# Kernel optimization log

Hardware: AMD Instinct MI355X
Metric: run time of the kernel (lower is better)

The kernel has to match this reference:

```python
import jax, jax.numpy as jnp
import numpy as np

N = 50000      # num_nodes
R = 12         # num_relations
RL = 2 * R + 1 # relation slots in each RGCN layer
D = 128        # embedding_dim
H = 128        # hidden_layer_size
B = 4          # num_bases
E = 320000     # num_edges


def _xavier(key, shape):
    fan_in, fan_out = shape[-2], shape[-1]
    lim = np.sqrt(6.0 / (fan_in + fan_out)).astype(np.float32)
    return jax.random.uniform(key, shape, jnp.float32, -lim, lim)


def setup_inputs() -> dict:
    key = jax.random.key(0)
    ks = jax.random.split(key, 12)
    edge_index = jax.random.randint(ks[0], (2, E), 0, N)
    edge_type = jax.random.randint(ks[1], (E,), 0, R)
    neg_tail = jax.random.randint(ks[2], (E,), 0, N)  # corrupted tails for BCE loss
    entity_embedding = _xavier(ks[3], (N, D))
    entity_bias = jnp.zeros((1, D), jnp.float32)
    bases1 = _xavier(ks[4], (B, D, H))
    comp1 = _xavier(ks[5], (RL, B))
    bias1 = jnp.zeros((H,), jnp.float32)
    bases2 = _xavier(ks[6], (B, H, D))
    comp2 = _xavier(ks[7], (RL, B))
    bias2 = jnp.zeros((D,), jnp.float32)
    rel_emb = _xavier(ks[8], (R, D))
    return {
        "entity_embedding": entity_embedding, "entity_bias": entity_bias,
        "bases1": bases1, "comp1": comp1, "bias1": bias1,
        "bases2": bases2, "comp2": comp2, "bias2": bias2,
        "rel_emb": rel_emb,
        "edge_index": edge_index, "edge_type": edge_type, "neg_tail": neg_tail,
    }


def rgcn_layer(x, edge_index, edge_type, bases, comp, bias):
    # Basis-decomposed relational conv: W_r = sum_b comp[r,b] * bases[b]
    # Project once through bases, then combine per-edge with comp[edge_type].
    src, dst = edge_index[0], edge_index[1]
    hb = jnp.einsum('ni,bio->nbo', x, bases)            # [N, B, out]
    c = comp[edge_type]                                  # [E, B]
    msg = jnp.einsum('eb,ebo->eo', c, hb[src])           # [E, out]
    n_edges = edge_type.shape[0]
    deg = jax.ops.segment_sum(jnp.ones((n_edges,), x.dtype), dst, num_segments=N)
    agg = jax.ops.segment_sum(msg, dst, num_segments=N)  # scatter-add aggregation
    return agg / jnp.maximum(deg, 1.0)[:, None] + bias


def reference(entity_embedding, entity_bias, bases1, comp1, bias1,
              bases2, comp2, bias2, rel_emb, edge_index, edge_type, neg_tail):
    x = jax.nn.relu(entity_embedding + entity_bias)
    x = jax.nn.relu(rgcn_layer(x, edge_index, edge_type, bases1, comp1, bias1))
    x = rgcn_layer(x, edge_index, edge_type, bases2, comp2, bias2)
    # DistMult decoding over the graph triples (h, r, t)
    h, t = edge_index[0], edge_index[1]
    re = rel_emb[edge_type]                              # [E, D]
    pred_logits = jnp.sum(x[h] * re * x[t], axis=-1)     # [E]
    neg_logits = jnp.sum(x[h] * re * x[neg_tail], axis=-1)
    loss = 0.5 * (jnp.mean(-jax.nn.log_sigmoid(pred_logits))
                  + jnp.mean(-jax.nn.log_sigmoid(-neg_logits)))
    roc_auc = jnp.mean((pred_logits > neg_logits).astype(jnp.float32))
    return pred_logits, loss, roc_auc
```

## Files before the change

kernel.cpp:

```cpp
#include <hip/hip_runtime.h>

typedef unsigned short ushort_t;
typedef __attribute__((ext_vector_type(8))) short short8;
typedef __attribute__((ext_vector_type(4))) float f32x4;

#define N_NODES 50000
#define NBASE   4
#define N_EDGE  320000
#define DM_BLOCKS 2048
#define N_GROUPS (N_EDGE / 8)
#define SCAN_BLOCKS 49
#define LDSB_STRIDE 136
#define FILL_B (N_EDGE / 256)
#define X0_B   (N_NODES * 128 / 256)

#define C_COMP1 0
#define C_COMP2 100
#define C_BIAS1 200
#define C_BIAS2 328
#define C_REL   456
#define C_EBIAS 1992
#define C_TOTAL 2120

__device__ __forceinline__ float bf2f(ushort_t u) {
    union { unsigned int i; float f; } v; v.i = ((unsigned int)u) << 16; return v.f;
}
__device__ __forceinline__ ushort_t f2bf(float f) {
    union { float f; unsigned int i; } v; v.f = f;
    unsigned int u = v.i;
    u = (u + 0x7FFFu + ((u >> 16) & 1u)) >> 16;
    return (ushort_t)u;
}
__device__ __forceinline__ float readf(const void* p, int i, int isbf) {
    return isbf ? bf2f(((const ushort_t*)p)[i]) : ((const float*)p)[i];
}
__device__ __forceinline__ float softplus(float x) {
    if (x > 20.f) return x;
    if (x < -20.f) return expf(x);
    return log1pf(expf(x));
}

__global__ void k_prepcnt(const ushort_t* __restrict__ emb, int* __restrict__ flag,
                          const void* comp1, const void* comp2, const void* b1, const void* b2,
                          const void* rel, const void* eb, float* __restrict__ canon,
                          const int* __restrict__ ei, int* __restrict__ cnt) {
    if (blockIdx.x == 0) {
        __shared__ int c;
        if (threadIdx.x == 0) c = 0;
        __syncthreads();
        int e = (emb[threadIdx.x] >> 7) & 0xFF;
        if (e >= 100 && e <= 126) atomicAdd(&c, 1);
        __syncthreads();
        if (threadIdx.x == 0) *flag = (c >= 200) ? 1 : 0;
        int isbf = (c >= 200) ? 1 : 0;
        for (int i = threadIdx.x; i < C_TOTAL; i += blockDim.x) {
            float v;
            if      (i < C_COMP2) v = readf(comp1, i - C_COMP1, isbf);
            else if (i < C_BIAS1) v = readf(comp2, i - C_COMP2, isbf);
            else if (i < C_BIAS2) v = readf(b1,    i - C_BIAS1, isbf);
            else if (i < C_REL)   v = readf(b2,    i - C_BIAS2, isbf);
            else if (i < C_EBIAS) v = readf(rel,   i - C_REL,   isbf);
            else                  v = readf(eb,    i - C_EBIAS, isbf);
            canon[i] = v;
        }
    } else {
        int e = (blockIdx.x - 1) * 256 + threadIdx.x;
        if (e < N_EDGE) atomicAdd(&cnt[ei[N_EDGE + e]], 1);
    }
}

__global__ void k_scan1(const int* __restrict__ cnt, int* __restrict__ ptr,
                        int* __restrict__ bsum) {
    __shared__ int s[1024];
    int t = threadIdx.x;
    int i = blockIdx.x * 1024 + t;
    int v = (i < N_NODES) ? cnt[i] : 0;
    s[t] = v;
    __syncthreads();
    for (int off = 1; off < 1024; off <<= 1) {
        int u = (t >= off) ? s[t - off] : 0;
        __syncthreads();
        s[t] += u;
        __syncthreads();
    }
    if (i < N_NODES) ptr[i] = s[t] - v;
    if (t == 1023) bsum[blockIdx.x] = s[1023];
}

__global__ void k_scan2(const int* __restrict__ bsum, int* __restrict__ boff) {
    int t = threadIdx.x;
    int v = (t < SCAN_BLOCKS) ? bsum[t] : 0;
    int orig = v;
    #pragma unroll
    for (int off = 1; off < 64; off <<= 1) {
        int u = __shfl_up(v, off);
        if (t >= off) v += u;
    }
    boff[t] = v - orig;
}

__global__ void k_scan3(int* __restrict__ ptr, int* __restrict__ cursor,
                        const int* __restrict__ boff) {
    int t = threadIdx.x;
    int i = blockIdx.x * 1024 + t;
    if (i < N_NODES) {
        int p = ptr[i] + boff[blockIdx.x];
        ptr[i] = p;
        cursor[i] = p;
    }
    if (blockIdx.x == 0 && t == 0) ptr[N_NODES] = N_EDGE;
}

__global__ void k_fillinit(const int* __restrict__ ei, const int* __restrict__ et,
                           int* __restrict__ cursor, unsigned int* __restrict__ packed,
                           const void* __restrict__ bases1, ushort_t* __restrict__ btK1,
                           const void* __restrict__ bases2, ushort_t* __restrict__ btK2,
                           const void* __restrict__ emb, const float* __restrict__ canon,
                           ushort_t* __restrict__ x, const int* __restrict__ flag) {
    int bid = blockIdx.x;
    if (bid < FILL_B) {
        int e = bid * 256 + threadIdx.x;
        int dst = ei[N_EDGE + e];
        int pos = atomicAdd(&cursor[dst], 1);
        packed[pos] = (unsigned int)(ei[e] & 0xFFFF) | ((unsigned int)et[e] << 16);
    } else if (bid < FILL_B + 512) {
        int isbf = *flag;
        int rb = bid - FILL_B;
        const void* bases = (rb < 256) ? bases1 : bases2;
        ushort_t* btK = (rb < 256) ? btK1 : btK2;
        int idx = (rb & 255) * 256 + threadIdx.x;
        int b = idx >> 14, i = (idx >> 7) & 127, o = idx & 127;
        btK[(size_t)o * 512 + (b << 7) + i] = f2bf(readf(bases, idx, isbf));
    } else {
        int isbf = *flag;
        int i = (bid - FILL_B - 512) * 256 + threadIdx.x;
        if (i < N_NODES * 128) {
            float v = readf(emb, i, isbf) + canon[C_EBIAS + (i & 127)];
            x[i] = f2bf(fmaxf(v, 0.f));
        }
    }
}

__global__ void k_agg2(const ushort_t* __restrict__ x, const int* __restrict__ ptr,
                       const unsigned int* __restrict__ packed, const float* __restrict__ compf,
                       ushort_t* __restrict__ y) {
    __shared__ float sc[100];
    int tid = threadIdx.x;
    for (int i = tid; i < 100; i += 256) sc[i] = compf[i];
    __syncthreads();
    int m = blockIdx.x * 4 + (tid >> 6);
    int lane = tid & 63;
    int o2 = lane << 1;
    int beg = ptr[m], end = ptr[m + 1];
    float l0 = 0.f, l1 = 0.f, l2 = 0.f, l3 = 0.f;
    float h0 = 0.f, h1 = 0.f, h2 = 0.f, h3 = 0.f;
    int i = beg;
    for (; i + 8 <= end; i += 8) {
        unsigned int p[8], wv[8];
        #pragma unroll
        for (int j = 0; j < 8; ++j) p[j] = packed[i + j];
        #pragma unroll
        for (int j = 0; j < 8; ++j)
            wv[j] = *(const unsigned int*)(x + (size_t)(p[j] & 0xFFFFu) * 128 + o2);
        #pragma unroll
        for (int j = 0; j < 8; ++j) {
            const float* c = sc + (p[j] >> 16) * 4;
            float vl = bf2f((ushort_t)wv[j]), vh = bf2f((ushort_t)(wv[j] >> 16));
            l0 += c[0] * vl; l1 += c[1] * vl; l2 += c[2] * vl; l3 += c[3] * vl;
            h0 += c[0] * vh; h1 += c[1] * vh; h2 += c[2] * vh; h3 += c[3] * vh;
        }
    }
    for (; i < end; ++i) {
        unsigned int p0 = packed[i];
        unsigned int w0 = *(const unsigned int*)(x + (size_t)(p0 & 0xFFFFu) * 128 + o2);
        const float* c0 = sc + (p0 >> 16) * 4;
        float vl = bf2f((ushort_t)w0), vh = bf2f((ushort_t)(w0 >> 16));
        l0 += c0[0] * vl; l1 += c0[1] * vl; l2 += c0[2] * vl; l3 += c0[3] * vl;
        h0 += c0[0] * vh; h1 += c0[1] * vh; h2 += c0[2] * vh; h3 += c0[3] * vh;
    }
    unsigned int* yp = (unsigned int*)(y + (size_t)m * 512 + o2);
    yp[0]   = (unsigned int)f2bf(l0) | ((unsigned int)f2bf(h0) << 16);
    yp[64]  = (unsigned int)f2bf(l1) | ((unsigned int)f2bf(h1) << 16);
    yp[128] = (unsigned int)f2bf(l2) | ((unsigned int)f2bf(h2) << 16);
    yp[192] = (unsigned int)f2bf(l3) | ((unsigned int)f2bf(h3) << 16);
}

__global__ __launch_bounds__(256) void
k_gemm512(const ushort_t* __restrict__ y, const ushort_t* __restrict__ btK,
          const int* __restrict__ cnt, const float* __restrict__ canon,
          ushort_t* __restrict__ xout, int cbias, int dorelu) {
    __shared__ ushort_t bs[128 * LDSB_STRIDE];
    int tid = threadIdx.x;
    int lane = tid & 63, w = tid >> 6;
    int r = lane & 15, q = lane >> 4;
    int m0 = blockIdx.x * 128;
    f32x4 acc[2][8] = {};
    int row0 = m0 + w * 32 + r;
    int row1 = row0 + 16;
    int cr0 = (row0 < N_NODES) ? row0 : (N_NODES - 1);
    int cr1 = (row1 < N_NODES) ? row1 : (N_NODES - 1);
    const ushort_t* ar0 = y + (size_t)cr0 * 512;
    const ushort_t* ar1 = y + (size_t)cr1 * 512;

    for (int c = 0; c < 4; ++c) {
        __syncthreads();
        {
            int o = tid >> 4;
            int j = (tid & 15) << 3;
            #pragma unroll
            for (int s = 0; s < 8; ++s, o += 16) {
                short8 v = *(const short8*)(btK + (size_t)o * 512 + c * 128 + j);
                *(short8*)(bs + o * LDSB_STRIDE + j) = v;
            }
        }
        __syncthreads();
        #pragma unroll
        for (int ksl = 0; ksl < 4; ++ksl) {
            int k0 = ksl * 32 + q * 8;
            short8 a0 = *(const short8*)(ar0 + c * 128 + k0);
            short8 a1 = *(const short8*)(ar1 + c * 128 + k0);
            #pragma unroll
            for (int t = 0; t < 8; ++t) {
                short8 b = *(const short8*)(bs + (t * 16 + r) * LDSB_STRIDE + k0);
                acc[0][t] = __builtin_amdgcn_mfma_f32_16x16x32_bf16(a0, b, acc[0][t], 0, 0, 0);
                acc[1][t] = __builtin_amdgcn_mfma_f32_16x16x32_bf16(a1, b, acc[1][t], 0, 0, 0);
            }
        }
    }
    #pragma unroll
    for (int i = 0; i < 2; ++i) {
        int rbase = m0 + w * 32 + i * 16 + (q << 2);
        float d[4];
        #pragma unroll
        for (int ii = 0; ii < 4; ++ii) {
            int rr = rbase + ii;
            d[ii] = fmaxf((float)cnt[(rr < N_NODES) ? rr : (N_NODES - 1)], 1.0f);
        }
        #pragma unroll
        for (int t = 0; t < 8; ++t) {
            int col = t * 16 + r;
            float bb = canon[cbias + col];
            #pragma unroll
            for (int ii = 0; ii < 4; ++ii) {
                int rr = rbase + ii;
                if (rr < N_NODES) {
                    float v = acc[i][t][ii] / d[ii] + bb;
                    if (dorelu) v = fmaxf(v, 0.f);
                    xout[(size_t)rr * 128 + col] = f2bf(v);
                }
            }
        }
    }
}

__global__ void k_distmult8b(const ushort_t* __restrict__ x2, const float* __restrict__ canon,
                             const int* __restrict__ ei, const int* __restrict__ et,
                             const int* __restrict__ neg, float* __restrict__ outp,
                             float* __restrict__ partials) {
    __shared__ float srel[1536];
    int tid = threadIdx.x;
    for (int i = tid; i < 1536; i += 256) srel[i] = canon[C_REL + i];
    __syncthreads();
    int lane = tid & 63;
    int g = lane >> 3;
    int l = lane & 7;
    int w = (blockIdx.x * blockDim.x + tid) >> 6;
    int nw = (DM_BLOCKS * 256) >> 6;
    float aL1 = 0.f, aL2 = 0.f, aA = 0.f;
    for (int gid = w; gid < N_GROUPS; gid += nw) {
        int e = gid * 8 + g;
        int h = ei[e], t = ei[N_EDGE + e], r = et[e], qn = neg[e];
        const ushort_t* ph = x2 + (size_t)h * 128 + l * 16;
        const ushort_t* pt = x2 + (size_t)t * 128 + l * 16;
        const ushort_t* pq = x2 + (size_t)qn * 128 + l * 16;
        const float*    pr = srel + r * 128 + l * 16;
        short8 h0 = *(const short8*)ph, h1 = *(const short8*)(ph + 8);
        short8 t0 = *(const short8*)pt, t1 = *(const short8*)(pt + 8);
        short8 q0 = *(const short8*)pq, q1 = *(const short8*)(pq + 8);
        float sp = 0.f, sn = 0.f;
        #pragma unroll
        for (int j = 0; j < 8; ++j) {
            float hv = bf2f(((const ushort_t*)&h0)[j]) * pr[j];
            sp += hv * bf2f(((const ushort_t*)&t0)[j]);
            sn += hv * bf2f(((const ushort_t*)&q0)[j]);
        }
        #pragma unroll
        for (int j = 0; j < 8; ++j) {
            float hv = bf2f(((const ushort_t*)&h1)[j]) * pr[8 + j];
            sp += hv * bf2f(((const ushort_t*)&t1)[j]);
            sn += hv * bf2f(((const ushort_t*)&q1)[j]);
        }
        sp += __shfl_down(sp, 4); sn += __shfl_down(sn, 4);
        sp += __shfl_down(sp, 2); sn += __shfl_down(sn, 2);
        sp += __shfl_down(sp, 1); sn += __shfl_down(sn, 1);
        if (l == 0) {
            outp[e] = sp;
            aL1 += softplus(-sp);
            aL2 += softplus(sn);
            aA  += (sp > sn) ? 1.0f : 0.0f;
        }
    }
    #pragma unroll
    for (int off = 32; off; off >>= 1) {
        aL1 += __shfl_down(aL1, off);
        aL2 += __shfl_down(aL2, off);
        aA  += __shfl_down(aA,  off);
    }
    __shared__ float s[3][4];
    int wl = tid >> 6;
    if (lane == 0) { s[0][wl] = aL1; s[1][wl] = aL2; s[2][wl] = aA; }
    __syncthreads();
    if (tid == 0) {
        float t0 = 0.f, t1 = 0.f, t2 = 0.f;
        for (int i = 0; i < 4; ++i) { t0 += s[0][i]; t1 += s[1][i]; t2 += s[2][i]; }
        partials[blockIdx.x * 3 + 0] = t0;
        partials[blockIdx.x * 3 + 1] = t1;
        partials[blockIdx.x * 3 + 2] = t2;
    }
}

__global__ void k_final(const float* __restrict__ partials, float* __restrict__ outp) {
    __shared__ float s[3][256];
    int tid = threadIdx.x;
    float t0 = 0.f, t1 = 0.f, t2 = 0.f;
    for (int i = tid; i < DM_BLOCKS; i += 256) {
        t0 += partials[i * 3 + 0];
        t1 += partials[i * 3 + 1];
        t2 += partials[i * 3 + 2];
    }
    s[0][tid] = t0; s[1][tid] = t1; s[2][tid] = t2;
    __syncthreads();
    for (int st = 128; st; st >>= 1) {
        if (tid < st) {
            s[0][tid] += s[0][tid + st];
            s[1][tid] += s[1][tid + st];
            s[2][tid] += s[2][tid + st];
        }
        __syncthreads();
    }
    if (tid == 0) {
        float inv = 1.0f / (float)N_EDGE;
        outp[N_EDGE]     = 0.5f * (s[0][0] * inv + s[1][0] * inv);
        outp[N_EDGE + 1] = s[2][0] * inv;
    }
}

extern "C" void kernel_launch(void* const* d_in, const int* in_sizes, int n_in,
                              void* d_out, int out_size, void* d_ws, size_t ws_size,
                              hipStream_t stream) {
    const void* emb    = d_in[0];
    const void* ebias  = d_in[1];
    const void* bases1 = d_in[2];
    const void* comp1  = d_in[3];
    const void* bias1  = d_in[4];
    const void* bases2 = d_in[5];
    const void* comp2  = d_in[6];
    const void* bias2  = d_in[7];
    const void* rel    = d_in[8];
    const int*  ei     = (const int*)d_in[9];
    const int*  et     = (const int*)d_in[10];
    const int*  neg    = (const int*)d_in[11];
    float*      outp   = (float*)d_out;

    char* ws = (char*)d_ws;
    size_t off = 0;
    auto alloc = [&](size_t bytes) { char* p = ws + off; off += (bytes + 255) & ~(size_t)255; return p; };
    int*          flag   = (int*)alloc(256);
    float*        canon  = (float*)alloc((size_t)C_TOTAL * 4);
    int*          cnt    = (int*)alloc((size_t)N_NODES * 4);
    int*          ptr    = (int*)alloc((size_t)(N_NODES + 1) * 4);
    int*          cursor = (int*)alloc((size_t)N_NODES * 4);
    int*          bsum   = (int*)alloc(SCAN_BLOCKS * 4);
    int*          boff   = (int*)alloc(64 * 4);
    ushort_t*     btK1   = (ushort_t*)alloc((size_t)128 * 512 * 2);
    ushort_t*     btK2   = (ushort_t*)alloc((size_t)128 * 512 * 2);
    float*        part   = (float*)alloc((size_t)DM_BLOCKS * 3 * 4);
    unsigned int* packed = (unsigned int*)alloc((size_t)N_EDGE * 4);
    ushort_t*     x      = (ushort_t*)alloc((size_t)N_NODES * 128 * 2);
    ushort_t*     y      = (ushort_t*)alloc((size_t)N_NODES * 512 * 2);

    hipMemsetAsync(cnt, 0, (size_t)N_NODES * 4, stream);
    k_prepcnt<<<1 + FILL_B, 256, 0, stream>>>((const ushort_t*)emb, flag, comp1, comp2,
                                              bias1, bias2, rel, ebias, canon, ei, cnt);
    k_scan1<<<SCAN_BLOCKS, 1024, 0, stream>>>(cnt, ptr, bsum);
    k_scan2<<<1, 64, 0, stream>>>(bsum, boff);
    k_scan3<<<SCAN_BLOCKS, 1024, 0, stream>>>(ptr, cursor, boff);
    k_fillinit<<<FILL_B + 512 + X0_B, 256, 0, stream>>>(ei, et, cursor, packed,
                                                        bases1, btK1, bases2, btK2,
                                                        emb, canon, x, flag);

    int ggrid = (N_NODES + 127) / 128;

    k_agg2<<<N_NODES / 4, 256, 0, stream>>>(x, ptr, packed, canon + C_COMP1, y);
    k_gemm512<<<ggrid, 256, 0, stream>>>(y, btK1, cnt, canon, x, C_BIAS1, 1);

    k_agg2<<<N_NODES / 4, 256, 0, stream>>>(x, ptr, packed, canon + C_COMP2, y);
    k_gemm512<<<ggrid, 256, 0, stream>>>(y, btK2, cnt, canon, x, C_BIAS2, 0);

    k_distmult8b<<<DM_BLOCKS, 256, 0, stream>>>(x, canon, ei, et, neg, outp, part);
    k_final<<<1, 256, 0, stream>>>(part, outp);
}
```

Before: 283.0 us.

## Fuse edge aggregation with basis GEMM, keep intermediate in shared memory

Combines the per-node basis-weighted aggregation and the 512-wide basis projection GEMM into one kernel. Each block aggregates 16 nodes into a shared-memory tile, then runs MFMA against the basis matrix read directly from global memory. This removes the 50000x512 bf16 intermediate round trip through HBM and one launch per layer, and ping-pongs between two node buffers. The cost is that each wave now handles the edges of 4 nodes with a per-edge branch to pick the accumulator, and every block re-reads the full basis matrix from global/L2 without LDS staging.

New measurement: 321.6 us. 13.7% more time.

```diff
diff --git a/kernel.cpp b/kernel.cpp
--- a/kernel.cpp
+++ b/kernel.cpp
@@ -10,9 +10,9 @@
 #define DM_BLOCKS 2048
 #define N_GROUPS (N_EDGE / 8)
 #define SCAN_BLOCKS 49
-#define LDSB_STRIDE 136
 #define FILL_B (N_EDGE / 256)
 #define X0_B   (N_NODES * 128 / 256)
+#define Y_STRIDE 520
 
 #define C_COMP1 0
 #define C_COMP2 100
@@ -141,114 +141,102 @@
     }
 }
 
-__global__ void k_agg2(const ushort_t* __restrict__ x, const int* __restrict__ ptr,
-                       const unsigned int* __restrict__ packed, const float* __restrict__ compf,
-                       ushort_t* __restrict__ y) {
+#define UPD(A)                                                        \
+    { A[0] += c[0] * vl; A[1] += c[1] * vl; A[2] += c[2] * vl;        \
+      A[3] += c[3] * vl; A[4] += c[0] * vh; A[5] += c[1] * vh;        \
+      A[6] += c[2] * vh; A[7] += c[3] * vh; }
+
+__global__ __launch_bounds__(256) void
+k_aggemm(const ushort_t* __restrict__ xin, const int* __restrict__ ptr,
+         const unsigned int* __restrict__ packed, const float* __restrict__ compf,
+         const ushort_t* __restrict__ btK, const int* __restrict__ cnt,
+         const float* __restrict__ canon, ushort_t* __restrict__ xout,
+         int cbias, int dorelu) {
+    __shared__ ushort_t ys[16 * Y_STRIDE];
     __shared__ float sc[100];
     int tid = threadIdx.x;
     for (int i = tid; i < 100; i += 256) sc[i] = compf[i];
     __syncthreads();
-    int m = blockIdx.x * 4 + (tid >> 6);
-    int lane = tid & 63;
+    int lane = tid & 63, w = tid >> 6;
+    int m0 = blockIdx.x * 16;
+    int n0 = m0 + w * 4;
     int o2 = lane << 1;
-    int beg = ptr[m], end = ptr[m + 1];
-    float l0 = 0.f, l1 = 0.f, l2 = 0.f, l3 = 0.f;
-    float h0 = 0.f, h1 = 0.f, h2 = 0.f, h3 = 0.f;
-    int i = beg;
-    for (; i + 8 <= end; i += 8) {
+    int e0 = ptr[n0], e1 = ptr[n0 + 1], e2 = ptr[n0 + 2],
+        e3 = ptr[n0 + 3], e4 = ptr[n0 + 4];
+    float acc[4][8] = {};
+    int i = e0;
+    for (; i + 8 <= e4; i += 8) {
         unsigned int p[8], wv[8];
         #pragma unroll
         for (int j = 0; j < 8; ++j) p[j] = packed[i + j];
         #pragma unroll
         for (int j = 0; j < 8; ++j)
-            wv[j] = *(const unsigned int*)(x + (size_t)(p[j] & 0xFFFFu) * 128 + o2);
+            wv[j] = *(const unsigned int*)(xin + (size_t)(p[j] & 0xFFFFu) * 128 + o2);
         #pragma unroll
         for (int j = 0; j < 8; ++j) {
             const float* c = sc + (p[j] >> 16) * 4;
             float vl = bf2f((ushort_t)wv[j]), vh = bf2f((ushort_t)(wv[j] >> 16));
-            l0 += c[0] * vl; l1 += c[1] * vl; l2 += c[2] * vl; l3 += c[3] * vl;
-            h0 += c[0] * vh; h1 += c[1] * vh; h2 += c[2] * vh; h3 += c[3] * vh;
-        }
-    }
-    for (; i < end; ++i) {
+            int idx = i + j;
+            int sel = (idx >= e1) + (idx >= e2) + (idx >= e3);
+            switch (sel) {
+            case 0:  UPD(acc[0]); break;
+            case 1:  UPD(acc[1]); break;
+            case 2:  UPD(acc[2]); break;
+            default: UPD(acc[3]); break;
+            }
+        }
+    }
+    for (; i < e4; ++i) {
         unsigned int p0 = packed[i];
-        unsigned int w0 = *(const unsigned int*)(x + (size_t)(p0 & 0xFFFFu) * 128 + o2);
-        const float* c0 = sc + (p0 >> 16) * 4;
+        unsigned int w0 = *(const unsigned int*)(xin + (size_t)(p0 & 0xFFFFu) * 128 + o2);
+        const float* c = sc + (p0 >> 16) * 4;
         float vl = bf2f((ushort_t)w0), vh = bf2f((ushort_t)(w0 >> 16));
-        l0 += c0[0] * vl; l1 += c0[1] * vl; l2 += c0[2] * vl; l3 += c0[3] * vl;
-        h0 += c0[0] * vh; h1 += c0[1] * vh; h2 += c0[2] * vh; h3 += c0[3] * vh;
-    }
-    unsigned int* yp = (unsigned int*)(y + (size_t)m * 512 + o2);
-    yp[0]   = (unsigned int)f2bf(l0) | ((unsigned int)f2bf(h0) << 16);
-    yp[64]  = (unsigned int)f2bf(l1) | ((unsigned int)f2bf(h1) << 16);
-    yp[128] = (unsigned int)f2bf(l2) | ((unsigned int)f2bf(h2) << 16);
-    yp[192] = (unsigned int)f2bf(l3) | ((unsigned int)f2bf(h3) << 16);
-}
-
-__global__ __launch_bounds__(256) void
-k_gemm512(const ushort_t* __restrict__ y, const ushort_t* __restrict__ btK,
-          const int* __restrict__ cnt, const float* __restrict__ canon,
-          ushort_t* __restrict__ xout, int cbias, int dorelu) {
-    __shared__ ushort_t bs[128 * LDSB_STRIDE];
-    int tid = threadIdx.x;
-    int lane = tid & 63, w = tid >> 6;
+        int sel = (i >= e1) + (i >= e2) + (i >= e3);
+        switch (sel) {
+        case 0:  UPD(acc[0]); break;
+        case 1:  UPD(acc[1]); break;
+        case 2:  UPD(acc[2]); break;
+        default: UPD(acc[3]); break;
+        }
+    }
+    unsigned int* yd = (unsigned int*)ys;
+    #pragma unroll
+    for (int n = 0; n < 4; ++n) {
+        int row = w * 4 + n;
+        #pragma unroll
+        for (int b = 0; b < 4; ++b)
+            yd[row * (Y_STRIDE / 2) + b * 64 + lane] =
+                (unsigned int)f2bf(acc[n][b]) | ((unsigned int)f2bf(acc[n][4 + b]) << 16);
+    }
+    __syncthreads();
+
     int r = lane & 15, q = lane >> 4;
-    int m0 = blockIdx.x * 128;
-    f32x4 acc[2][8] = {};
-    int row0 = m0 + w * 32 + r;
-    int row1 = row0 + 16;
-    int cr0 = (row0 < N_NODES) ? row0 : (N_NODES - 1);
-    int cr1 = (row1 < N_NODES) ? row1 : (N_NODES - 1);
-    const ushort_t* ar0 = y + (size_t)cr0 * 512;
-    const ushort_t* ar1 = y + (size_t)cr1 * 512;
-
-    for (int c = 0; c < 4; ++c) {
-        __syncthreads();
-        {
-            int o = tid >> 4;
-            int j = (tid & 15) << 3;
-            #pragma unroll
-            for (int s = 0; s < 8; ++s, o += 16) {
-                short8 v = *(const short8*)(btK + (size_t)o * 512 + c * 128 + j);
-                *(short8*)(bs + o * LDSB_STRIDE + j) = v;
-            }
-        }
-        __syncthreads();
-        #pragma unroll
-        for (int ksl = 0; ksl < 4; ++ksl) {
-            int k0 = ksl * 32 + q * 8;
-            short8 a0 = *(const short8*)(ar0 + c * 128 + k0);
-            short8 a1 = *(const short8*)(ar1 + c * 128 + k0);
-            #pragma unroll
-            for (int t = 0; t < 8; ++t) {
-                short8 b = *(const short8*)(bs + (t * 16 + r) * LDSB_STRIDE + k0);
-                acc[0][t] = __builtin_amdgcn_mfma_f32_16x16x32_bf16(a0, b, acc[0][t], 0, 0, 0);
-                acc[1][t] = __builtin_amdgcn_mfma_f32_16x16x32_bf16(a1, b, acc[1][t], 0, 0, 0);
-            }
-        }
-    }
-    #pragma unroll
-    for (int i = 0; i < 2; ++i) {
-        int rbase = m0 + w * 32 + i * 16 + (q << 2);
-        float d[4];
+    f32x4 dacc[2] = {};
+    const ushort_t* arow = ys + r * Y_STRIDE;
+    #pragma unroll
+    for (int ks = 0; ks < 16; ++ks) {
+        int k0 = ks * 32 + q * 8;
+        short8 a = *(const short8*)(arow + k0);
+        #pragma unroll
+        for (int cf = 0; cf < 2; ++cf) {
+            int col = w * 32 + cf * 16 + r;
+            short8 b = *(const short8*)(btK + (size_t)col * 512 + k0);
+            dacc[cf] = __builtin_amdgcn_mfma_f32_16x16x32_bf16(a, b, dacc[cf], 0, 0, 0);
+        }
+    }
+    int rbase = m0 + (q << 2);
+    float d[4];
+    #pragma unroll
+    for (int ii = 0; ii < 4; ++ii) d[ii] = fmaxf((float)cnt[rbase + ii], 1.0f);
+    #pragma unroll
+    for (int cf = 0; cf < 2; ++cf) {
+        int col = w * 32 + cf * 16 + r;
+        float bb = canon[cbias + col];
         #pragma unroll
         for (int ii = 0; ii < 4; ++ii) {
-            int rr = rbase + ii;
-            d[ii] = fmaxf((float)cnt[(rr < N_NODES) ? rr : (N_NODES - 1)], 1.0f);
-        }
-        #pragma unroll
-        for (int t = 0; t < 8; ++t) {
-            int col = t * 16 + r;
-            float bb = canon[cbias + col];
-            #pragma unroll
-            for (int ii = 0; ii < 4; ++ii) {
-                int rr = rbase + ii;
-                if (rr < N_NODES) {
-                    float v = acc[i][t][ii] / d[ii] + bb;
-                    if (dorelu) v = fmaxf(v, 0.f);
-                    xout[(size_t)rr * 128 + col] = f2bf(v);
-                }
-            }
+            float v = dacc[cf][ii] / d[ii] + bb;
+            if (dorelu) v = fmaxf(v, 0.f);
+            xout[(size_t)(rbase + ii) * 128 + col] = f2bf(v);
         }
     }
 }
@@ -376,8 +364,8 @@
     ushort_t*     btK2   = (ushort_t*)alloc((size_t)128 * 512 * 2);
     float*        part   = (float*)alloc((size_t)DM_BLOCKS * 3 * 4);
     unsigned int* packed = (unsigned int*)alloc((size_t)N_EDGE * 4);
-    ushort_t*     x      = (ushort_t*)alloc((size_t)N_NODES * 128 * 2);
-    ushort_t*     y      = (ushort_t*)alloc((size_t)N_NODES * 512 * 2);
+    ushort_t*     xA     = (ushort_t*)alloc((size_t)N_NODES * 128 * 2);
+    ushort_t*     xB     = (ushort_t*)alloc((size_t)N_NODES * 128 * 2);
 
     hipMemsetAsync(cnt, 0, (size_t)N_NODES * 4, stream);
     k_prepcnt<<<1 + FILL_B, 256, 0, stream>>>((const ushort_t*)emb, flag, comp1, comp2,
@@ -387,16 +375,13 @@
     k_scan3<<<SCAN_BLOCKS, 1024, 0, stream>>>(ptr, cursor, boff);
     k_fillinit<<<FILL_B + 512 + X0_B, 256, 0, stream>>>(ei, et, cursor, packed,
                                                         bases1, btK1, bases2, btK2,
-                                                        emb, canon, x, flag);
-
-    int ggrid = (N_NODES + 127) / 128;
-
-    k_agg2<<<N_NODES / 4, 256, 0, stream>>>(x, ptr, packed, canon + C_COMP1, y);
-    k_gemm512<<<ggrid, 256, 0, stream>>>(y, btK1, cnt, canon, x, C_BIAS1, 1);
-
-    k_agg2<<<N_NODES / 4, 256, 0, stream>>>(x, ptr, packed, canon + C_COMP2, y);
-    k_gemm512<<<ggrid, 256, 0, stream>>>(y, btK2, cnt, canon, x, C_BIAS2, 0);
-
-    k_distmult8b<<<DM_BLOCKS, 256, 0, stream>>>(x, canon, ei, et, neg, outp, part);
+                                                        emb, canon, xA, flag);
+
+    k_aggemm<<<N_NODES / 16, 256, 0, stream>>>(xA, ptr, packed, canon + C_COMP1,
+                                               btK1, cnt, canon, xB, C_BIAS1, 1);
+    k_aggemm<<<N_NODES / 16, 256, 0, stream>>>(xB, ptr, packed, canon + C_COMP2,
+                                               btK2, cnt, canon, xA, C_BIAS2, 0);
+
+    k_distmult8b<<<DM_BLOCKS, 256, 0, stream>>>(xA, canon, ei, et, neg, outp, part);
     k_final<<<1, 256, 0, stream>>>(part, outp);
 }
```
